# Kernel tuning notes

Measured on AMD Instinct MI355X. Metric: run time of the kernel, lower is better.

## Reference

```python
import jax, jax.numpy as jnp
import numpy as np

DECAY = 0.99
EPS = 1e-5


def setup_inputs() -> dict:
    key = jax.random.key(0)
    k1, k2 = jax.random.split(key)
    inp = jax.random.normal(k1, (32, 64, 64, 64), dtype=jnp.float32)  # [B,H,W,dim]
    embed = jax.random.normal(k2, (64, 512), dtype=jnp.float32)       # [dim, n_embed]
    cluster_size = jnp.zeros((512,), dtype=jnp.float32)
    embed_avg = embed  # buffer initialized as embed.clone() in torch
    return {"input": inp, "embed": embed, "cluster_size": cluster_size, "embed_avg": embed_avg}


def reference(input, embed, cluster_size, embed_avg):
    dim, n_embed = embed.shape
    flatten = input.reshape(-1, dim)  # [N, dim]

    # pairwise squared distances via ||f||^2 - 2 f.E + ||E||^2 -> [N, n_embed]
    dist = ((flatten ** 2).sum(1, keepdims=True)
            - 2.0 * flatten @ embed
            + (embed ** 2).sum(0, keepdims=True))
    embed_ind_flat = jnp.argmin(dist, axis=1)  # [N] (== argmax of -dist)

    # codebook lookup (F.embedding on embed.T)
    quantize = jnp.take(embed.T, embed_ind_flat, axis=0).reshape(input.shape)

    # EMA stats: one-hot sum and one-hot @ flatten expressed as scatter-adds
    ones = jnp.ones_like(embed_ind_flat, dtype=flatten.dtype)
    embed_onehot_sum = jax.ops.segment_sum(ones, embed_ind_flat, num_segments=n_embed)      # [n_embed]
    embed_sum = jax.ops.segment_sum(flatten, embed_ind_flat, num_segments=n_embed).T       # [dim, n_embed]

    new_cluster_size = cluster_size * DECAY + (1.0 - DECAY) * embed_onehot_sum
    new_embed_avg = embed_avg * DECAY + (1.0 - DECAY) * embed_sum
    n = new_cluster_size.sum()
    cs = (new_cluster_size + EPS) / (n + n_embed * EPS) * n
    new_embed = new_embed_avg / cs[None, :]

    diff = ((jax.lax.stop_gradient(quantize) - input) ** 2).mean()
    quantize_st = input + jax.lax.stop_gradient(quantize - input)  # straight-through
    embed_ind = embed_ind_flat.reshape(input.shape[:-1])

    return (quantize_st, diff, embed_ind, new_cluster_size, new_embed_avg, new_embed)
```

## Files before the change

kernel.cpp:

```cpp
#include <hip/hip_runtime.h>

typedef __attribute__((ext_vector_type(8))) short short8_t;
typedef __attribute__((ext_vector_type(4))) float f32x4;

#define N_ROWS   131072
#define DIM      64
#define NE       512
#define DECAYF   0.99f
#define OMDECAY  0.01f
#define EPSF     1e-5f
#define GAP_THR  0.02f

#define Q_OFF    0
#define DIFF_OFF 8388608
#define IND_OFF  8388609
#define CS_OFF   8519681
#define AVG_OFF  8520193
#define EMB_OFF  8552961

#define WS_ET      0
#define WS_ENORM   32768
#define WS_EN64    33280
#define WS_CSDIV   34304
#define WS_DIFF    34816
#define WS_RCNT    34817
#define WS_IDX     34818
#define WS_RLIST   165890
#define WS_BH      296964
#define WS_BL      313348
#define WS_HIST    329732
#define WS_BINBASE 330244
#define WS_CURSOR  330756
#define WS_SORTED  331268
#define WS_ACCUM   462340

__device__ __forceinline__ ushort f32_to_bf16_rn(float f) {
    unsigned u = __float_as_uint(f);
    unsigned r = (u + 0x7FFFu + ((u >> 16) & 1u)) >> 16;
    return (ushort)r;
}
__device__ __forceinline__ float bf16_to_f32(ushort h) {
    return __uint_as_float(((unsigned)h) << 16);
}

__global__ __launch_bounds__(64) void prep_kernel(const float* __restrict__ embed,
                                                  float* __restrict__ ws) {
    const int c = blockIdx.x;
    const int d = threadIdx.x;
    float v = embed[d * NE + c];
    ws[WS_ET + c * DIM + d] = v;

    ushort hb = f32_to_bf16_rn(v);
    float  lf = v - bf16_to_f32(hb);
    ushort lb = f32_to_bf16_rn(lf);

    const int T  = c >> 4;
    const int n  = c & 15;
    const int s  = d >> 5;
    const int k8 = (d >> 3) & 3;
    const int jj = d & 7;
    const int l  = k8 * 16 + n;
    const int idx = (T * 2 + s) * 512 + l * 8 + jj;
    ((ushort*)(ws + WS_BH))[idx] = hb;
    ((ushort*)(ws + WS_BL))[idx] = lb;

    double sq = (double)v * (double)v;
    #pragma unroll
    for (int off = 32; off > 0; off >>= 1) sq += __shfl_down(sq, off, 64);
    if (d == 0) {
        ws[WS_ENORM + c] = (float)sq;
        ((double*)(ws + WS_EN64))[c] = sq;
        ((int*)ws)[WS_HIST + c] = 0;
        if (c == 0) {
            ws[WS_DIFF] = 0.0f;
            ((int*)ws)[WS_RCNT] = 0;
        }
    }
    ws[WS_ACCUM + c * DIM + d] = 0.0f;
}

__global__ __launch_bounds__(256) void dist_kernel(const float* __restrict__ input,
                                                   float* __restrict__ ws) {
    const int tid  = threadIdx.x;
    const int lane = tid & 63;
    const int wv   = tid >> 6;
    const int r0   = blockIdx.x * 128 + wv * 32;
    const int n15  = lane & 15;
    const int koff = (lane >> 4) * 8;

    short8_t Ahi[2][2], Alo[2][2];
    #pragma unroll
    for (int sub = 0; sub < 2; sub++) {
        const float* rp = input + (size_t)(r0 + sub * 16 + n15) * DIM + koff;
        #pragma unroll
        for (int s = 0; s < 2; s++) {
            float4 x0 = *(const float4*)(rp + s * 32);
            float4 x1 = *(const float4*)(rp + s * 32 + 4);
            float xf[8] = {x0.x, x0.y, x0.z, x0.w, x1.x, x1.y, x1.z, x1.w};
            short8_t h, l;
            #pragma unroll
            for (int e = 0; e < 8; e++) {
                ushort hb = f32_to_bf16_rn(xf[e]);
                float  lf = xf[e] - bf16_to_f32(hb);
                ushort lb = f32_to_bf16_rn(lf);
                h[e] = (short)hb;
                l[e] = (short)lb;
            }
            Ahi[sub][s] = h;
            Alo[sub][s] = l;
        }
    }

    const ushort* bhp = (const ushort*)(ws + WS_BH) + lane * 8;
    const ushort* blp = (const ushort*)(ws + WS_BL) + lane * 8;

    float m1[8], m2[8];
    int   j1[8];
    #pragma unroll
    for (int i = 0; i < 8; i++) { m1[i] = 3.4e38f; m2[i] = 3.4e38f; j1[i] = 0; }

    #pragma unroll 2
    for (int T = 0; T < 32; T++) {
        short8_t Bh0 = *(const short8_t*)(bhp + T * 1024);
        short8_t Bh1 = *(const short8_t*)(bhp + T * 1024 + 512);
        short8_t Bl0 = *(const short8_t*)(blp + T * 1024);
        short8_t Bl1 = *(const short8_t*)(blp + T * 1024 + 512);

        f32x4 aa = {0.f, 0.f, 0.f, 0.f};
        f32x4 ab = {0.f, 0.f, 0.f, 0.f};
        aa = __builtin_amdgcn_mfma_f32_16x16x32_bf16(Ahi[0][0], Bh0, aa, 0, 0, 0);
        ab = __builtin_amdgcn_mfma_f32_16x16x32_bf16(Ahi[1][0], Bh0, ab, 0, 0, 0);
        aa = __builtin_amdgcn_mfma_f32_16x16x32_bf16(Alo[0][0], Bh0, aa, 0, 0, 0);
        ab = __builtin_amdgcn_mfma_f32_16x16x32_bf16(Alo[1][0], Bh0, ab, 0, 0, 0);
        aa = __builtin_amdgcn_mfma_f32_16x16x32_bf16(Ahi[0][0], Bl0, aa, 0, 0, 0);
        ab = __builtin_amdgcn_mfma_f32_16x16x32_bf16(Ahi[1][0], Bl0, ab, 0, 0, 0);
        aa = __builtin_amdgcn_mfma_f32_16x16x32_bf16(Ahi[0][1], Bh1, aa, 0, 0, 0);
        ab = __builtin_amdgcn_mfma_f32_16x16x32_bf16(Ahi[1][1], Bh1, ab, 0, 0, 0);
        aa = __builtin_amdgcn_mfma_f32_16x16x32_bf16(Alo[0][1], Bh1, aa, 0, 0, 0);
        ab = __builtin_amdgcn_mfma_f32_16x16x32_bf16(Alo[1][1], Bh1, ab, 0, 0, 0);
        aa = __builtin_amdgcn_mfma_f32_16x16x32_bf16(Ahi[0][1], Bl1, aa, 0, 0, 0);
        ab = __builtin_amdgcn_mfma_f32_16x16x32_bf16(Ahi[1][1], Bl1, ab, 0, 0, 0);

        const float en = ws[WS_ENORM + T * 16 + n15];
        const int   jc = T * 16 + n15;
        #pragma unroll
        for (int q = 0; q < 4; q++) {
            float da = fmaf(-2.0f, aa[q], en);
            m2[q]    = fminf(m2[q], fmaxf(m1[q], da));
            j1[q]    = (da < m1[q]) ? jc : j1[q];
            m1[q]    = fminf(m1[q], da);
            float db = fmaf(-2.0f, ab[q], en);
            m2[q+4]  = fminf(m2[q+4], fmaxf(m1[q+4], db));
            j1[q+4]  = (db < m1[q+4]) ? jc : j1[q+4];
            m1[q+4]  = fminf(m1[q+4], db);
        }
    }

    #pragma unroll
    for (int off = 1; off < 16; off <<= 1) {
        #pragma unroll
        for (int i = 0; i < 8; i++) {
            float b1 = __shfl_xor(m1[i], off, 64);
            float b2 = __shfl_xor(m2[i], off, 64);
            int   bj = __shfl_xor(j1[i], off, 64);
            float a1 = m1[i];
            float nm2 = fminf(fminf(m2[i], b2), fmaxf(a1, b1));
            bool takeB = (b1 < a1) || (b1 == a1 && bj < j1[i]);
            m1[i] = takeB ? b1 : a1;
            j1[i] = takeB ? bj : j1[i];
            m2[i] = nm2;
        }
    }

    if (n15 == 0) {
        #pragma unroll
        for (int i = 0; i < 8; i++) {
            int sub = i >> 2, q = i & 3;
            int r = r0 + sub * 16 + (lane >> 4) * 4 + q;
            ((int*)ws)[WS_IDX + r] = j1[i];
            if (m2[i] - m1[i] < GAP_THR) {
                int pos = atomicAdd((int*)ws + WS_RCNT, 1);
                ((int*)ws)[WS_RLIST + pos] = r;
            }
        }
    }
}

__global__ __launch_bounds__(256) void refine_kernel(const float* __restrict__ input,
                                                     float* __restrict__ ws) {
    __shared__ float rowf[4][DIM];
    const int cnt  = ((const int*)ws)[WS_RCNT];
    const int lane = threadIdx.x & 63;
    const int wv   = threadIdx.x >> 6;
    const double* en64 = (const double*)(ws + WS_EN64);

    for (int ii = blockIdx.x * 4 + wv; ii < cnt; ii += 2048) {
        const int r = ((const int*)ws)[WS_RLIST + ii];
        rowf[wv][lane] = input[(size_t)r * DIM + lane];
        double bd = 1e300;
        int    bj = 0x7fffffff;
        for (int kk = 0; kk < 8; kk++) {
            int j = kk * 64 + lane;
            const float* ep = ws + WS_ET + j * DIM;
            double s0 = 0.0, s1 = 0.0;
            #pragma unroll 8
            for (int d = 0; d < DIM; d += 2) {
                s0 = fma((double)ep[d],     (double)rowf[wv][d],     s0);
                s1 = fma((double)ep[d + 1], (double)rowf[wv][d + 1], s1);
            }
            double dist = en64[j] - 2.0 * (s0 + s1);
            if (dist < bd || (dist == bd && j < bj)) { bd = dist; bj = j; }
        }
        #pragma unroll
        for (int off = 32; off > 0; off >>= 1) {
            double od = __shfl_down(bd, off, 64);
            int    oj = __shfl_down(bj, off, 64);
            if (od < bd || (od == bd && oj < bj)) { bd = od; bj = oj; }
        }
        if (lane == 0) ((int*)ws)[WS_IDX + r] = bj;
    }
}

__global__ __launch_bounds__(256) void hist_kernel(float* __restrict__ ws) {
    __shared__ int hist[NE];
    const int tid = threadIdx.x;
    for (int e = tid; e < NE; e += 256) hist[e] = 0;
    __syncthreads();

    const int4 j4 = *((const int4*)((const int*)ws + WS_IDX) + blockIdx.x * 256 + tid);
    atomicAdd(&hist[j4.x], 1);
    atomicAdd(&hist[j4.y], 1);
    atomicAdd(&hist[j4.z], 1);
    atomicAdd(&hist[j4.w], 1);
    __syncthreads();

    for (int e = tid; e < NE; e += 256) {
        int h = hist[e];
        if (h) atomicAdd((int*)ws + WS_HIST + e, h);
    }
}

__global__ __launch_bounds__(512) void scanfin_kernel(const float* __restrict__ cluster_size,
                                                      float* __restrict__ ws,
                                                      float* __restrict__ out) {
    __shared__ int wsums[8];
    __shared__ float red[8];
    const int t    = threadIdx.x;
    const int lane = t & 63;
    const int wv   = t >> 6;
    const int v    = ((const int*)ws)[WS_HIST + t];
    const float csnew = fmaf(cluster_size[t], DECAYF, OMDECAY * (float)v);
    out[CS_OFF + t] = csnew;

    int x = v;
    #pragma unroll
    for (int off = 1; off < 64; off <<= 1) {
        int y = __shfl_up(x, off, 64);
        if (lane >= off) x += y;
    }
    if (lane == 63) wsums[wv] = x;

    float s = csnew;
    #pragma unroll
    for (int off = 32; off > 0; off >>= 1) s += __shfl_down(s, off, 64);
    if (lane == 0) red[wv] = s;
    __syncthreads();

    int add = 0;
    for (int w = 0; w < wv; w++) add += wsums[w];
    const int excl = x + add - v;
    ((int*)ws)[WS_BINBASE + t] = excl;
    ((int*)ws)[WS_CURSOR + t]  = excl;

    float n = red[0] + red[1] + red[2] + red[3] + red[4] + red[5] + red[6] + red[7];
    ws[WS_CSDIV + t] = (csnew + EPSF) / (n + (float)NE * EPSF) * n;
}

__global__ __launch_bounds__(256) void place_kernel(float* __restrict__ ws) {
    __shared__ int lhist[NE];
    __shared__ int lbase[NE];
    __shared__ int lcur[NE];
    const int tid  = threadIdx.x;
    const int base = blockIdx.x * 256;

    for (int e = tid; e < NE; e += 256) { lhist[e] = 0; lcur[e] = 0; }
    __syncthreads();

    const int r = base + tid;
    const int j = ((const int*)ws)[WS_IDX + r];
    atomicAdd(&lhist[j], 1);
    __syncthreads();

    for (int e = tid; e < NE; e += 256)
        if (lhist[e]) lbase[e] = atomicAdd((int*)ws + WS_CURSOR + e, lhist[e]);
    __syncthreads();

    const int pos = lbase[j] + atomicAdd(&lcur[j], 1);
    ((int*)ws)[WS_SORTED + pos] = r;
}

__global__ __launch_bounds__(256) void sum_kernel(const float* __restrict__ input,
                                                  float* __restrict__ ws,
                                                  float* __restrict__ out) {
    __shared__ float wred[4];
    const int lane = threadIdx.x & 63;
    const int wv   = threadIdx.x >> 6;
    const int i0   = (blockIdx.x * 4 + wv) * 32;

    const int rv = ((const int*)ws)[WS_SORTED + i0 + (lane & 31)];
    const int jv = ((const int*)ws)[WS_IDX + rv];

    float acc  = 0.0f;
    float dacc = 0.0f;
    int   jcur = __shfl(jv, 0, 64);

    #pragma unroll
    for (int k = 0; k < 32; k += 8) {
        int   rr[8], jj[8];
        float v[8], q[8];
        #pragma unroll
        for (int u = 0; u < 8; u++) {
            rr[u] = __shfl(rv, k + u, 64);
            jj[u] = __shfl(jv, k + u, 64);
        }
        #pragma unroll
        for (int u = 0; u < 8; u++) v[u] = input[(size_t)rr[u] * DIM + lane];
        #pragma unroll
        for (int u = 0; u < 8; u++) q[u] = ws[WS_ET + jj[u] * DIM + lane];

        #pragma unroll
        for (int u = 0; u < 8; u++) {
            out[Q_OFF + (size_t)rr[u] * DIM + lane] = q[u];
            float dd = q[u] - v[u];
            dacc = fmaf(dd, dd, dacc);
            if (lane == 0) out[IND_OFF + rr[u]] = (float)jj[u];
            if (jj[u] != jcur) {
                atomicAdd(&ws[WS_ACCUM + jcur * DIM + lane], acc);
                acc = 0.0f;
                jcur = jj[u];
            }
            acc += v[u];
        }
    }
    atomicAdd(&ws[WS_ACCUM + jcur * DIM + lane], acc);

    #pragma unroll
    for (int off = 1; off < 64; off <<= 1) dacc += __shfl_xor(dacc, off, 64);
    if (lane == 0) wred[wv] = dacc;
    __syncthreads();
    if (threadIdx.x == 0)
        atomicAdd(&ws[WS_DIFF], wred[0] + wred[1] + wred[2] + wred[3]);
}

__global__ __launch_bounds__(512) void emaout_kernel(const float* __restrict__ embed_avg,
                                                     const float* __restrict__ ws,
                                                     float* __restrict__ out) {
    const int e = blockIdx.x * 512 + threadIdx.x;
    const int d = e >> 9;
    const int j = e & (NE - 1);
    float s   = ws[WS_ACCUM + j * DIM + d];
    float avg = fmaf(embed_avg[e], DECAYF, OMDECAY * s);
    out[AVG_OFF + e] = avg;
    out[EMB_OFF + e] = avg / ws[WS_CSDIV + j];
    if (e == 0) out[DIFF_OFF] = ws[WS_DIFF] * (1.0f / 8388608.0f);
}

extern "C" void kernel_launch(void* const* d_in, const int* in_sizes, int n_in,
                              void* d_out, int out_size, void* d_ws, size_t ws_size,
                              hipStream_t stream) {
    const float* input        = (const float*)d_in[0];
    const float* embed        = (const float*)d_in[1];
    const float* cluster_size = (const float*)d_in[2];
    const float* embed_avg    = (const float*)d_in[3];
    float* out = (float*)d_out;
    float* ws  = (float*)d_ws;

    prep_kernel<<<512, 64, 0, stream>>>(embed, ws);
    dist_kernel<<<N_ROWS / 128, 256, 0, stream>>>(input, ws);
    refine_kernel<<<512, 256, 0, stream>>>(input, ws);
    hist_kernel<<<128, 256, 0, stream>>>(ws);
    scanfin_kernel<<<1, 512, 0, stream>>>(cluster_size, ws, out);
    place_kernel<<<512, 256, 0, stream>>>(ws);
    sum_kernel<<<N_ROWS / 128, 256, 0, stream>>>(input, ws, out);
    emaout_kernel<<<64, 512, 0, stream>>>(embed_avg, ws, out);
}
```

Before: 116.3 us.

## Split codebook across wave pairs in dist kernel and merge top-2 via LDS

Each block now covers 64 rows instead of 128. Each pair of waves shares the same 32 rows, and the two waves of a pair each scan half of the 512 codewords. Per-row best and second-best distances are combined through shared memory by one wave before the index is written and the near-tie row is queued. This doubles the grid and halves the serial loop per wave to expose more parallelism. The cost is that each row's A operand is loaded and split twice, plus an added __syncthreads and LDS merge.

```diff
diff --git a/kernel.cpp b/kernel.cpp
--- a/kernel.cpp
+++ b/kernel.cpp
@@ -81,12 +81,19 @@
 
 __global__ __launch_bounds__(256) void dist_kernel(const float* __restrict__ input,
                                                    float* __restrict__ ws) {
+    __shared__ float m1s[4][32];
+    __shared__ float m2s[4][32];
+    __shared__ int   j1s[4][32];
+
     const int tid  = threadIdx.x;
     const int lane = tid & 63;
     const int wv   = tid >> 6;
-    const int r0   = blockIdx.x * 128 + wv * 32;
+    const int rowg = wv >> 1;
+    const int half = wv & 1;
+    const int r0   = blockIdx.x * 64 + rowg * 32;
     const int n15  = lane & 15;
-    const int koff = (lane >> 4) * 8;
+    const int k16  = lane >> 4;
+    const int koff = k16 * 8;
 
     short8_t Ahi[2][2], Alo[2][2];
     #pragma unroll
@@ -111,8 +118,9 @@
         }
     }
 
-    const ushort* bhp = (const ushort*)(ws + WS_BH) + lane * 8;
-    const ushort* blp = (const ushort*)(ws + WS_BL) + lane * 8;
+    const ushort* bhp = (const ushort*)(ws + WS_BH) + half * 16 * 1024 + lane * 8;
+    const ushort* blp = (const ushort*)(ws + WS_BL) + half * 16 * 1024 + lane * 8;
+    const int jbase = half * 256;
 
     float m1[8], m2[8];
     int   j1[8];
@@ -120,11 +128,11 @@
     for (int i = 0; i < 8; i++) { m1[i] = 3.4e38f; m2[i] = 3.4e38f; j1[i] = 0; }
 
     #pragma unroll 2
-    for (int T = 0; T < 32; T++) {
-        short8_t Bh0 = *(const short8_t*)(bhp + T * 1024);
-        short8_t Bh1 = *(const short8_t*)(bhp + T * 1024 + 512);
-        short8_t Bl0 = *(const short8_t*)(blp + T * 1024);
-        short8_t Bl1 = *(const short8_t*)(blp + T * 1024 + 512);
+    for (int t = 0; t < 16; t++) {
+        short8_t Bh0 = *(const short8_t*)(bhp + t * 1024);
+        short8_t Bh1 = *(const short8_t*)(bhp + t * 1024 + 512);
+        short8_t Bl0 = *(const short8_t*)(blp + t * 1024);
+        short8_t Bl1 = *(const short8_t*)(blp + t * 1024 + 512);
 
         f32x4 aa = {0.f, 0.f, 0.f, 0.f};
         f32x4 ab = {0.f, 0.f, 0.f, 0.f};
@@ -141,8 +149,8 @@
         aa = __builtin_amdgcn_mfma_f32_16x16x32_bf16(Ahi[0][1], Bl1, aa, 0, 0, 0);
         ab = __builtin_amdgcn_mfma_f32_16x16x32_bf16(Ahi[1][1], Bl1, ab, 0, 0, 0);
 
-        const float en = ws[WS_ENORM + T * 16 + n15];
-        const int   jc = T * 16 + n15;
+        const float en = ws[WS_ENORM + jbase + t * 16 + n15];
+        const int   jc = jbase + t * 16 + n15;
         #pragma unroll
         for (int q = 0; q < 4; q++) {
             float da = fmaf(-2.0f, aa[q], en);
@@ -176,12 +184,32 @@
         #pragma unroll
         for (int i = 0; i < 8; i++) {
             int sub = i >> 2, q = i & 3;
-            int r = r0 + sub * 16 + (lane >> 4) * 4 + q;
-            ((int*)ws)[WS_IDX + r] = j1[i];
-            if (m2[i] - m1[i] < GAP_THR) {
-                int pos = atomicAdd((int*)ws + WS_RCNT, 1);
-                ((int*)ws)[WS_RLIST + pos] = r;
-            }
+            int rl = sub * 16 + k16 * 4 + q;
+            m1s[wv][rl] = m1[i];
+            m2s[wv][rl] = m2[i];
+            j1s[wv][rl] = j1[i];
+        }
+    }
+    __syncthreads();
+
+    if (tid < 64) {
+        const int rg   = tid >> 5;
+        const int rl   = tid & 31;
+        const int pa   = rg * 2;
+        const float a1 = m1s[pa][rl],     b1 = m1s[pa + 1][rl];
+        const float a2 = m2s[pa][rl],     b2 = m2s[pa + 1][rl];
+        const int   ja = j1s[pa][rl],     jb = j1s[pa + 1][rl];
+
+        const bool  takeB = b1 < a1;
+        const float m1f = fminf(a1, b1);
+        const int   j1f = takeB ? jb : ja;
+        const float m2f = fminf(fminf(a2, b2), fmaxf(a1, b1));
+
+        const int r = blockIdx.x * 64 + rg * 32 + rl;
+        ((int*)ws)[WS_IDX + r] = j1f;
+        if (m2f - m1f < GAP_THR) {
+            int pos = atomicAdd((int*)ws + WS_RCNT, 1);
+            ((int*)ws)[WS_RLIST + pos] = r;
         }
     }
 }
@@ -376,7 +404,7 @@
     float* ws  = (float*)d_ws;
 
     prep_kernel<<<512, 64, 0, stream>>>(embed, ws);
-    dist_kernel<<<N_ROWS / 128, 256, 0, stream>>>(input, ws);
+    dist_kernel<<<N_ROWS / 64, 256, 0, stream>>>(input, ws);
     refine_kernel<<<512, 256, 0, stream>>>(input, ws);
     hist_kernel<<<128, 256, 0, stream>>>(ws);
     scanfin_kernel<<<1, 512, 0, stream>>>(cluster_size, ws, out);
```

New measurement: 120.7 us. +3.8%, slower.
